# Kernel optimization log

Measured on AMD Instinct MI355X. Metric: run time of the kernel, lower is better.

Reference implementation:

```python
import jax, jax.numpy as jnp
import numpy as np

B, CIN, COUT, L, K, D = 64, 128, 256, 1024, 3, 2
P = (K - 1) * D  # causal padding = 4
THRESH = 0.1
SLOPE = 0.2  # LeakyReLU negative slope


def setup_inputs() -> dict:
    key = jax.random.key(0)
    ks = jax.random.split(key, 24)
    rn = lambda k, shape, s=0.05: jax.random.normal(k, shape, dtype=jnp.float32) * s
    return {
        "x": rn(ks[0], (B, CIN, L), 1.0),
        "conv1_w": rn(ks[1], (COUT, CIN, K)),
        "conv1_b": rn(ks[2], (COUT,)),
        "Wz_w": rn(ks[3], (COUT, COUT)), "Wz_b": rn(ks[4], (COUT,)),
        "Uz_w": rn(ks[5], (COUT, COUT)), "Uz_b": rn(ks[6], (COUT,)),
        "Wr_w": rn(ks[7], (COUT, COUT)), "Wr_b": rn(ks[8], (COUT,)),
        "Ur_w": rn(ks[9], (COUT, COUT)), "Ur_b": rn(ks[10], (COUT,)),
        "Wh_w": rn(ks[11], (COUT, COUT)), "Wh_b": rn(ks[12], (COUT,)),
        "Uh_w": rn(ks[13], (COUT, COUT)), "Uh_b": rn(ks[14], (COUT,)),
        "conv2_w": rn(ks[15], (COUT, COUT, K)),
        "conv2_b": rn(ks[16], (COUT,)),
        "skip_w": rn(ks[17], (COUT, CIN, 1)),
        "skip_b": rn(ks[18], (COUT,)),
        "aw": jnp.ones((1,), jnp.float32),  # AttentionZeroedLayer param, init ones
    }


def _causal_conv(x, w, b):
    # x: [B,C,L], w: [O,I,K]; pad both sides by P then chomp the right tail
    y = jax.lax.conv_general_dilated(
        x, w, window_strides=(1,), padding=[(P, P)], rhs_dilation=(D,),
        dimension_numbers=("NCH", "OIH", "NCH"))
    y = y + b[None, :, None]
    return y[:, :, :-P] if P > 0 else y


def reference(x, conv1_w, conv1_b, Wz_w, Wz_b, Uz_w, Uz_b, Wr_w, Wr_b,
              Ur_w, Ur_b, Wh_w, Wh_b, Uh_w, Uh_b, conv2_w, conv2_b,
              skip_w, skip_b, aw):
    res = x
    # conv1 -> chomp -> LeakyReLU (dropout=0, identity in eval)
    h1 = jax.nn.leaky_relu(_causal_conv(x, conv1_w, conv1_b), SLOPE)  # [B,COUT,L]
    xt = h1.transpose(0, 2, 1)  # [B,L,C]
    # precompute input-side GRU projections as batched GEMMs
    xz = jnp.einsum("blc,hc->blh", xt, Wz_w) + Wz_b
    xr = jnp.einsum("blc,hc->blh", xt, Wr_w) + Wr_b
    xh = jnp.einsum("blc,hc->blh", xt, Wh_w) + Wh_b

    def step(h, ins):
        xz_t, xr_t, xh_t = ins
        z = jax.nn.sigmoid(xz_t + h @ Uz_w.T + Uz_b)
        r = jax.nn.sigmoid(xr_t + h @ Ur_w.T + Ur_b)
        h_tilde = jnp.tanh(xh_t + r * (h @ Uh_w.T + Uh_b))
        h_new = (1 - z) * h + z * h_tilde
        return h_new, h_new

    h0 = jnp.zeros((B, COUT), x.dtype)
    _, hs = jax.lax.scan(step, h0, (xz.transpose(1, 0, 2),
                                    xr.transpose(1, 0, 2),
                                    xh.transpose(1, 0, 2)))  # [L,B,C]
    g = hs.transpose(1, 2, 0)  # [B,COUT,L]
    # AttentionZeroedLayer: zero elements with |g| < threshold * sigmoid(aw)
    gate = jax.nn.sigmoid(aw)[0]
    g = jnp.where(jnp.abs(g) < THRESH * gate, jnp.zeros_like(g), g)
    # conv2 -> chomp -> LeakyReLU
    y = jax.nn.leaky_relu(_causal_conv(g, conv2_w, conv2_b), SLOPE)
    # 1x1 skip connection (in_channels != out_channels)
    res = jax.lax.conv_general_dilated(
        res, skip_w, window_strides=(1,), padding=[(0, 0)],
        dimension_numbers=("NCH", "OIH", "NCH")) + skip_b[None, :, None]
    return y + res
```

## Files before the change

### kernel.cpp

```cpp
#include <hip/hip_runtime.h>
#include <hip/hip_bf16.h>


typedef _Float16 f16;
typedef _Float16 h2_t __attribute__((ext_vector_type(2)));

__device__ __forceinline__ float bf1(unsigned short s){ return __uint_as_float(((unsigned)s)<<16); }

__device__ __forceinline__ unsigned packh2(float a, float b){
  h2_t h; h[0] = (f16)a; h[1] = (f16)b;
  return *(unsigned*)&h;
}
__device__ __forceinline__ unsigned bf2h2(unsigned u){
  return packh2(bf1((unsigned short)(u & 0xffffu)), bf1((unsigned short)(u >> 16)));
}

__device__ __forceinline__ float fdot2(unsigned a, unsigned b, float c){
#if __has_builtin(__builtin_amdgcn_fdot2)
  return __builtin_amdgcn_fdot2(*(h2_t*)&a, *(h2_t*)&b, c, false);
#else
  h2_t x = *(h2_t*)&a, y = *(h2_t*)&b;
  return c + (float)x[0]*(float)y[0] + (float)x[1]*(float)y[1];
#endif
}

__device__ __forceinline__ unsigned short f2bf(float f){
  __hip_bfloat16 h = __float2bfloat16(f);
  return *(unsigned short*)&h;
}
__device__ __forceinline__ unsigned packbf2(float a, float b){
  return (unsigned)f2bf(a) | ((unsigned)f2bf(b)<<16);
}
__device__ __forceinline__ float h2lo(unsigned u){ h2_t h = *(h2_t*)&u; return (float)h[0]; }
__device__ __forceinline__ float h2hi(unsigned u){ h2_t h = *(h2_t*)&u; return (float)h[1]; }

__device__ __forceinline__ bool aw_is_f32(const void* aw){
  return ((const unsigned*)aw)[0] == 0x3F800000u;
}

__device__ __forceinline__ float dpp_add_b1(float v){
  int x = __builtin_amdgcn_update_dpp(0, __float_as_int(v), 0xB1, 0xF, 0xF, true);
  return v + __int_as_float(x);
}
__device__ __forceinline__ float dpp_add_4e(float v){
  int x = __builtin_amdgcn_update_dpp(0, __float_as_int(v), 0x4E, 0xF, 0xF, true);
  return v + __int_as_float(x);
}
__device__ __forceinline__ float red4(float v){
  return dpp_add_4e(dpp_add_b1(v));
}

__global__ void k_repack(const void* __restrict__ w1,  const void* __restrict__ w2,
                         const void* __restrict__ Wz,  const void* __restrict__ Wr,
                         const void* __restrict__ Wh,  const void* __restrict__ wsk,
                         const void* __restrict__ Uz,  const void* __restrict__ Ur,
                         const void* __restrict__ Uh,
                         const void* __restrict__ b1,  const void* __restrict__ Wzb,
                         const void* __restrict__ Wrb, const void* __restrict__ Whb,
                         const void* __restrict__ Uzb, const void* __restrict__ Urb,
                         const void* __restrict__ Uhb, const void* __restrict__ b2,
                         const void* __restrict__ bsk, const void* __restrict__ aw,
                         f16* __restrict__ p1, f16* __restrict__ p2,
                         f16* __restrict__ pz, f16* __restrict__ pr,
                         f16* __restrict__ ph, f16* __restrict__ ps,
                         f16* __restrict__ puz, f16* __restrict__ pur,
                         f16* __restrict__ puh, float* __restrict__ bc)
{
  const bool f32 = aw_is_f32(aw);
  auto G = [&](const void* p, int idx)->float{
    return f32 ? ((const float*)p)[idx] : bf1(((const unsigned short*)p)[idx]);
  };
  int i = blockIdx.x*256 + threadIdx.x;
  if (i < 196608){
    int t=i/65536, r=i%65536, cc=r>>11, r2=r&2047, o=r2>>3, ci=r2&7, c=cc*8+ci;
    p2[i] = (f16)G(w2, o*768 + c*3 + t);
  }
  if (i < 98304){
    int t=i/32768, r=i%32768, cc=r>>11, r2=r&2047, o=r2>>3, ci=r2&7, c=cc*8+ci;
    p1[i] = (f16)G(w1, o*384 + c*3 + t);
  }
  if (i < 65536){
    int cc=i>>11, r2=i&2047, o=r2>>3, ci=r2&7, c=cc*8+ci;
    int s = o*256 + c;
    pz[i]=(f16)G(Wz, s); pr[i]=(f16)G(Wr, s); ph[i]=(f16)G(Wh, s);
    puz[i]=(f16)G(Uz, i); pur[i]=(f16)G(Ur, i); puh[i]=(f16)G(Uh, i);
  }
  if (i < 32768){
    int cc=i>>11, r2=i&2047, o=r2>>3, ci=r2&7, c=cc*8+ci;
    ps[i]=(f16)G(wsk, o*128 + c);
  }
  if (i < 2304){
    int which = i>>8, j = i&255;
    const void* src[9] = {b1, Wzb, Wrb, Whb, Uzb, Urb, Uhb, b2, bsk};
    bc[i] = G(src[which], j);
  }
  if (i == 2304){
    float v = G(aw, 0);
    bc[2304] = 0.1f / (1.f + __expf(-v));
    bc[2305] = f32 ? 1.f : 0.f;
  }
}

__global__ __launch_bounds__(256,2) void k_conv1proj(
    const void* __restrict__ x,
    const f16* __restrict__ W1,
    const f16* __restrict__ WZ, const f16* __restrict__ WR, const f16* __restrict__ WH,
    const float* __restrict__ bc,
    f16* __restrict__ XZ, f16* __restrict__ XR, f16* __restrict__ XH,
    int Lc, int t0)
{
  __shared__ unsigned smem_u[12544];
  f16* xa = (f16*)smem_u;
  unsigned* tileA = smem_u + 4352;
  f16* hy = (f16*)(smem_u + 4352);
  const int b = blockIdx.y;
  const int lt = blockIdx.x*64;
  const int gl0 = t0 + lt;
  const int tid = threadIdx.x, lb = tid&7, ob = tid>>3;
  const bool f32 = (bc[2305] != 0.f);

  #pragma unroll
  for (int k=0;k<17;k++){
    int idx = tid + k*256;
    int c = idx/34, lp = idx - c*34;
    int gl = gl0 - 4 + lp*2;
    unsigned u = 0u;
    if (gl >= 0){
      if (f32){
        float2 v = *(const float2*)((const float*)x + ((size_t)b*128 + c)*1024 + gl);
        u = packh2(v.x, v.y);
      } else {
        u = bf2h2(*(const unsigned*)((const unsigned short*)x + ((size_t)b*128 + c)*1024 + gl));
      }
    }
    tileA[c*35 + lp] = u;
  }
  __syncthreads();
  #pragma unroll
  for (int k=0;k<17;k++){
    int idx = tid + k*256;
    int row = idx>>6, cp = idx&63;
    unsigned u0 = tileA[(2*cp)*35 + (row>>1)];
    unsigned u1 = tileA[(2*cp+1)*35 + (row>>1)];
    unsigned short s0 = (row&1)? (unsigned short)(u0>>16):(unsigned short)(u0&0xffffu);
    unsigned short s1 = (row&1)? (unsigned short)(u1>>16):(unsigned short)(u1&0xffffu);
    int sw = (cp>>2) ^ ((row>>3)&7);
    *(unsigned*)(&xa[row*128 + sw*8 + (cp&3)*2]) = (unsigned)s0 | ((unsigned)s1<<16);
  }
  __syncthreads();

  float acc[8][8];
  uint4 wreg[8], wnext[8];

  #pragma unroll
  for (int i=0;i<8;i++)
    #pragma unroll
    for (int j=0;j<8;j++) acc[i][j]=0.f;
  #pragma unroll
  for (int oi=0;oi<8;oi++) wreg[oi] = *(const uint4*)(W1 + ob*64 + oi*8);
  for (int ch=0; ch<48; ch++){
    if (ch+1 < 48){
      const f16* wn = W1 + (size_t)(ch+1)*2048 + ob*64;
      #pragma unroll
      for (int oi=0;oi<8;oi++) wnext[oi] = *(const uint4*)(wn + oi*8);
    }
    int t = ch>>4, cc = ch&15;
    #pragma unroll
    for (int li=0; li<8; li++){
      int row = lb*8 + li + t*2;
      int sw = cc ^ ((row>>3)&7);
      uint4 a = *(const uint4*)(&xa[row*128 + sw*8]);
      #pragma unroll
      for (int oi=0; oi<8; oi++){
        acc[li][oi] = fdot2(a.x, wreg[oi].x, acc[li][oi]);
        acc[li][oi] = fdot2(a.y, wreg[oi].y, acc[li][oi]);
        acc[li][oi] = fdot2(a.z, wreg[oi].z, acc[li][oi]);
        acc[li][oi] = fdot2(a.w, wreg[oi].w, acc[li][oi]);
      }
    }
    #pragma unroll
    for (int oi=0;oi<8;oi++) wreg[oi] = wnext[oi];
  }
  {
    const float* bp = bc + 0 + ob*8;
    #pragma unroll
    for (int li=0; li<8; li++){
      int row = lb*8 + li;
      f16 vals[8];
      #pragma unroll
      for (int oi=0;oi<8;oi++){
        float v = acc[li][oi] + bp[oi];
        vals[oi] = (f16)((v>0.f) ? v : 0.2f*v);
      }
      *(uint4*)(&hy[row*256 + ((ob ^ ((row>>3)&7))<<3)]) = *(uint4*)vals;
    }
  }
  __syncthreads();

  const f16* Wg[3] = {WZ, WR, WH};
  f16* Og[3] = {XZ, XR, XH};
  for (int g3=0; g3<3; g3++){
    const f16* Wp = Wg[g3];
    #pragma unroll
    for (int i=0;i<8;i++)
      #pragma unroll
      for (int j=0;j<8;j++) acc[i][j]=0.f;
    #pragma unroll
    for (int oi=0;oi<8;oi++) wreg[oi] = *(const uint4*)(Wp + ob*64 + oi*8);
    for (int ch=0; ch<32; ch++){
      if (ch+1 < 32){
        const f16* wn = Wp + (size_t)(ch+1)*2048 + ob*64;
        #pragma unroll
        for (int oi=0;oi<8;oi++) wnext[oi] = *(const uint4*)(wn + oi*8);
      }
      #pragma unroll
      for (int li=0; li<8; li++){
        int row = lb*8 + li;
        int sw = ch ^ ((row>>3)&7);
        uint4 a = *(const uint4*)(&hy[row*256 + sw*8]);
        #pragma unroll
        for (int oi=0; oi<8; oi++){
          acc[li][oi] = fdot2(a.x, wreg[oi].x, acc[li][oi]);
          acc[li][oi] = fdot2(a.y, wreg[oi].y, acc[li][oi]);
          acc[li][oi] = fdot2(a.z, wreg[oi].z, acc[li][oi]);
          acc[li][oi] = fdot2(a.w, wreg[oi].w, acc[li][oi]);
        }
      }
      #pragma unroll
      for (int oi=0;oi<8;oi++) wreg[oi] = wnext[oi];
    }
    f16* Ob = Og[g3] + ((size_t)b*Lc + lt)*256 + ob*8;
    #pragma unroll
    for (int li=0; li<8; li++){
      f16 vals[8];
      #pragma unroll
      for (int oi=0;oi<8;oi++){
        int o = ob*8 + oi;
        float bias = bc[256 + g3*256 + o] + ((g3<2) ? bc[1024 + g3*256 + o] : 0.f);
        vals[oi] = (f16)(acc[li][oi] + bias);
      }
      *(uint4*)(Ob + (size_t)(lb*8 + li)*256) = *(uint4*)vals;
    }
  }
}

__global__ __launch_bounds__(512)
__attribute__((amdgpu_waves_per_eu(2,2)))
void k_scan(
    const f16* __restrict__ XZ, const f16* __restrict__ XR, const f16* __restrict__ XH,
    const f16* __restrict__ pUz, const f16* __restrict__ pUr, const f16* __restrict__ pUh,
    const float* __restrict__ bc,
    f16* __restrict__ G, float* __restrict__ carry,
    int Lc, int first)
{
  const int b = blockIdx.x, tid = threadIdx.x;
  const int kp = tid&3, grp = tid>>2, r0 = grp*2;
  __shared__ unsigned hb[2][160];

  {
    f16* gb = G + (size_t)b*(Lc+4)*256;
    int row = tid>>7, col = tid&127;
    unsigned v = 0u;
    if (!first) v = *(unsigned*)(gb + (size_t)(Lc+row)*256 + col*2);
    *(unsigned*)(gb + (size_t)row*256 + col*2) = v;
  }

  unsigned uz0[32],uz1[32],ur0[32],ur1[32],uh0[32],uh1[32];
  const int cbase = kp*64;
  #pragma unroll
  for (int j4=0;j4<8;j4++){
    uint4 q;
    q = *(const uint4*)(pUz + r0*256     + cbase + j4*8);
    uz0[j4*4+0]=q.x; uz0[j4*4+1]=q.y; uz0[j4*4+2]=q.z; uz0[j4*4+3]=q.w;
    q = *(const uint4*)(pUz + (r0+1)*256 + cbase + j4*8);
    uz1[j4*4+0]=q.x; uz1[j4*4+1]=q.y; uz1[j4*4+2]=q.z; uz1[j4*4+3]=q.w;
    q = *(const uint4*)(pUr + r0*256     + cbase + j4*8);
    ur0[j4*4+0]=q.x; ur0[j4*4+1]=q.y; ur0[j4*4+2]=q.z; ur0[j4*4+3]=q.w;
    q = *(const uint4*)(pUr + (r0+1)*256 + cbase + j4*8);
    ur1[j4*4+0]=q.x; ur1[j4*4+1]=q.y; ur1[j4*4+2]=q.z; ur1[j4*4+3]=q.w;
    q = *(const uint4*)(pUh + r0*256     + cbase + j4*8);
    uh0[j4*4+0]=q.x; uh0[j4*4+1]=q.y; uh0[j4*4+2]=q.z; uh0[j4*4+3]=q.w;
    q = *(const uint4*)(pUh + (r0+1)*256 + cbase + j4*8);
    uh1[j4*4+0]=q.x; uh1[j4*4+1]=q.y; uh1[j4*4+2]=q.z; uh1[j4*4+3]=q.w;
  }
  const float bh0=bc[1536+r0], bh1=bc[1536+r0+1];
  const float thr = bc[2304];
  float hp0, hp1;
  if (first){ hp0 = 0.f; hp1 = 0.f; }
  else { hp0 = carry[b*256 + r0]; hp1 = carry[b*256 + r0 + 1]; }
  const int wslot = (grp>>5)*40 + (grp&31);
  if (kp == 0) hb[0][wslot] = packh2(hp0, hp1);

  const f16* xzp = XZ + (size_t)b*Lc*256 + r0;
  const f16* xrp = XR + (size_t)b*Lc*256 + r0;
  const f16* xhp = XH + (size_t)b*Lc*256 + r0;
  f16* gp = G + (size_t)b*(Lc+4)*256 + r0;

  unsigned xzv = *(const unsigned*)(xzp);
  unsigned xrv = *(const unsigned*)(xrp);
  unsigned xhv = *(const unsigned*)(xhp);
  __syncthreads();

  for (int t=0; t<Lc; t++){
    const int tn = (t+1 < Lc) ? t+1 : t;
    const unsigned nz = *(const unsigned*)(xzp + (size_t)tn*256);
    const unsigned nr = *(const unsigned*)(xrp + (size_t)tn*256);
    const unsigned nh = *(const unsigned*)(xhp + (size_t)tn*256);

    const unsigned* hbr = hb[t&1] + kp*40;
    float az0=0,az1=0,ar0=0,ar1=0,ah0=0,ah1=0;
    #pragma unroll
    for (int j4=0;j4<8;j4++){
      const uint4 hv = *(const uint4*)(hbr + j4*4);
      const unsigned hw[4] = {hv.x, hv.y, hv.z, hv.w};
      #pragma unroll
      for (int p=0;p<4;p++){
        const int J = j4*4+p;
        az0 = fdot2(hw[p], uz0[J], az0);
        az1 = fdot2(hw[p], uz1[J], az1);
        ar0 = fdot2(hw[p], ur0[J], ar0);
        ar1 = fdot2(hw[p], ur1[J], ar1);
        ah0 = fdot2(hw[p], uh0[J], ah0);
        ah1 = fdot2(hw[p], uh1[J], ah1);
      }
    }
    az0 = red4(az0); az1 = red4(az1);
    ar0 = red4(ar0); ar1 = red4(ar1);
    ah0 = red4(ah0); ah1 = red4(ah1);

    const float z0  = 1.f/(1.f+__expf(-(h2lo(xzv)+az0)));
    const float z1  = 1.f/(1.f+__expf(-(h2hi(xzv)+az1)));
    const float rr0 = 1.f/(1.f+__expf(-(h2lo(xrv)+ar0)));
    const float rr1 = 1.f/(1.f+__expf(-(h2hi(xrv)+ar1)));
    const float e0  = __expf(2.f*(h2lo(xhv)+rr0*(ah0+bh0)));
    const float e1  = __expf(2.f*(h2hi(xhv)+rr1*(ah1+bh1)));
    const float hh0 = 1.f - 2.f/(e0+1.f);
    const float hh1 = 1.f - 2.f/(e1+1.f);
    const float hn0 = (1.f-z0)*hp0 + z0*hh0;
    const float hn1 = (1.f-z1)*hp1 + z1*hh1;
    hp0 = hn0; hp1 = hn1;
    if (kp == 0){
      const float g0 = (fabsf(hn0) < thr) ? 0.f : hn0;
      const float g1 = (fabsf(hn1) < thr) ? 0.f : hn1;
      *(unsigned*)(gp + (size_t)(t+4)*256) = packh2(g0, g1);
      hb[(t+1)&1][wslot] = packh2(hn0, hn1);
    }
    xzv = nz; xrv = nr; xhv = nh;
    __syncthreads();
  }
  if (kp == 0){
    carry[b*256 + r0]     = hp0;
    carry[b*256 + r0 + 1] = hp1;
  }
}

__global__ __launch_bounds__(256,2) void k_final(const f16* __restrict__ G,
    const void* __restrict__ x, const f16* __restrict__ W2,
    const f16* __restrict__ WS, const float* __restrict__ bc,
    void* __restrict__ out, int Lc, int t0)
{
  __shared__ unsigned smem2[8704];
  f16* atG = (f16*)smem2;
  const int b = blockIdx.y;
  const int lt = blockIdx.x*64;
  const int gl0 = t0 + lt;
  const int tid = threadIdx.x, lb = tid&7, ob = tid>>3;
  const bool f32 = (bc[2305] != 0.f);

  {
    const f16* Ab = G + (size_t)b*(Lc+4)*256 + (size_t)lt*256;
    for (int idx=tid; idx<68*32; idx+=256){
      int row = idx>>5, cc = idx&31;
      uint4 v = *(const uint4*)(Ab + (size_t)row*256 + cc*8);
      *(uint4*)(&atG[row*256 + ((cc ^ ((row>>3)&7))<<3)]) = v;
    }
  }
  __syncthreads();

  float acc[8][8];
  #pragma unroll
  for (int i=0;i<8;i++)
    #pragma unroll
    for (int j=0;j<8;j++) acc[i][j]=0.f;

  uint4 wreg[8], wnext[8];
  #pragma unroll
  for (int oi=0;oi<8;oi++) wreg[oi] = *(const uint4*)(W2 + ob*64 + oi*8);
  for (int ch=0; ch<96; ch++){
    if (ch+1 < 96){
      const f16* wn = W2 + (size_t)(ch+1)*2048 + ob*64;
      #pragma unroll
      for (int oi=0;oi<8;oi++) wnext[oi] = *(const uint4*)(wn + oi*8);
    }
    int t = ch>>5, cc = ch&31;
    #pragma unroll
    for (int li=0; li<8; li++){
      int row = lb*8 + li + t*2;
      uint4 a = *(const uint4*)(&atG[row*256 + ((cc ^ ((row>>3)&7))<<3)]);
      #pragma unroll
      for (int oi=0; oi<8; oi++){
        acc[li][oi] = fdot2(a.x, wreg[oi].x, acc[li][oi]);
        acc[li][oi] = fdot2(a.y, wreg[oi].y, acc[li][oi]);
        acc[li][oi] = fdot2(a.z, wreg[oi].z, acc[li][oi]);
        acc[li][oi] = fdot2(a.w, wreg[oi].w, acc[li][oi]);
      }
    }
    #pragma unroll
    for (int oi=0;oi<8;oi++) wreg[oi] = wnext[oi];
  }
  {
    const float* bp = bc + 1792 + ob*8;
    #pragma unroll
    for (int li=0;li<8;li++)
      #pragma unroll
      for (int oi=0;oi<8;oi++){
        float v = acc[li][oi] + bp[oi];
        acc[li][oi] = (v>0.f) ? v : 0.2f*v;
      }
  }
  __syncthreads();

  unsigned* tileB = smem2;
  f16* xa2 = (f16*)(smem2 + 4352);
  #pragma unroll
  for (int k=0;k<16;k++){
    int idx = tid + k*256;
    int c = idx>>5, lp = idx&31;
    unsigned u;
    if (f32){
      float2 v = *(const float2*)((const float*)x + ((size_t)b*128 + c)*1024 + gl0 + lp*2);
      u = packh2(v.x, v.y);
    } else {
      u = bf2h2(*(const unsigned*)((const unsigned short*)x + ((size_t)b*128 + c)*1024 + gl0 + lp*2));
    }
    tileB[c*33 + lp] = u;
  }
  __syncthreads();
  #pragma unroll
  for (int k=0;k<16;k++){
    int idx = tid + k*256;
    int row = idx>>6, cp = idx&63;
    unsigned u0 = tileB[(2*cp)*33 + (row>>1)];
    unsigned u1 = tileB[(2*cp+1)*33 + (row>>1)];
    unsigned short s0 = (row&1)? (unsigned short)(u0>>16):(unsigned short)(u0&0xffffu);
    unsigned short s1 = (row&1)? (unsigned short)(u1>>16):(unsigned short)(u1&0xffffu);
    int sw = (cp>>2) ^ ((row>>3)&7);
    *(unsigned*)(&xa2[row*128 + sw*8 + (cp&3)*2]) = (unsigned)s0 | ((unsigned)s1<<16);
  }
  __syncthreads();

  #pragma unroll
  for (int oi=0;oi<8;oi++) wreg[oi] = *(const uint4*)(WS + ob*64 + oi*8);
  for (int ch=0; ch<16; ch++){
    if (ch+1 < 16){
      const f16* wn = WS + (size_t)(ch+1)*2048 + ob*64;
      #pragma unroll
      for (int oi=0;oi<8;oi++) wnext[oi] = *(const uint4*)(wn + oi*8);
    }
    #pragma unroll
    for (int li=0; li<8; li++){
      int row = lb*8 + li;
      int sw = ch ^ ((row>>3)&7);
      uint4 a = *(const uint4*)(&xa2[row*128 + sw*8]);
      #pragma unroll
      for (int oi=0; oi<8; oi++){
        acc[li][oi] = fdot2(a.x, wreg[oi].x, acc[li][oi]);
        acc[li][oi] = fdot2(a.y, wreg[oi].y, acc[li][oi]);
        acc[li][oi] = fdot2(a.z, wreg[oi].z, acc[li][oi]);
        acc[li][oi] = fdot2(a.w, wreg[oi].w, acc[li][oi]);
      }
    }
    #pragma unroll
    for (int oi=0;oi<8;oi++) wreg[oi] = wnext[oi];
  }
  {
    const float* sp = bc + 2048 + ob*8;
    #pragma unroll
    for (int oi=0;oi<8;oi++){
      int o = ob*8 + oi;
      size_t base = ((size_t)b*256 + o)*1024 + gl0 + lb*8;
      if (f32){
        float st[8];
        #pragma unroll
        for (int j=0;j<8;j++) st[j] = acc[j][oi] + sp[oi];
        *(uint4*)((float*)out + base)     = *(uint4*)&st[0];
        *(uint4*)((float*)out + base + 4) = *(uint4*)&st[4];
      } else {
        unsigned st[4];
        #pragma unroll
        for (int j=0;j<4;j++)
          st[j] = packbf2(acc[2*j][oi] + sp[oi], acc[2*j+1][oi] + sp[oi]);
        *(uint4*)((unsigned short*)out + base) = *(uint4*)st;
      }
    }
  }
}

extern "C" void kernel_launch(void* const* d_in, const int* in_sizes, int n_in,
                              void* d_out, int out_size, void* d_ws, size_t ws_size,
                              hipStream_t stream)
{
  const void* x   = d_in[0];
  const void* w1  = d_in[1];
  const void* b1  = d_in[2];
  const void* Wz  = d_in[3];
  const void* Wzb = d_in[4];
  const void* Uz  = d_in[5];
  const void* Uzb = d_in[6];
  const void* Wr  = d_in[7];
  const void* Wrb = d_in[8];
  const void* Ur  = d_in[9];
  const void* Urb = d_in[10];
  const void* Wh  = d_in[11];
  const void* Whb = d_in[12];
  const void* Uh  = d_in[13];
  const void* Uhb = d_in[14];
  const void* w2  = d_in[15];
  const void* b2  = d_in[16];
  const void* wsk = d_in[17];
  const void* bsk = d_in[18];
  const void* aw  = d_in[19];

  auto need = [](long long Lc)->size_t{
    return (size_t)(2LL*(758784LL + 3LL*64*Lc*256 + 64LL*(Lc+4)*256));
  };
  int Lc = 1024;
  if (ws_size < need(1024)) Lc = 256;
  if (ws_size < need(256))  Lc = 64;
  const int NCH = 1024 / Lc;

  f16* W = (f16*)d_ws;
  f16*   w1p   = W;
  f16*   w2p   = W + 98304;
  f16*   wzp   = W + 294912;
  f16*   wrp   = W + 360448;
  f16*   whp   = W + 425984;
  f16*   wsp   = W + 491520;
  f16*   uzp   = W + 524288;
  f16*   urp   = W + 589824;
  f16*   uhp   = W + 655360;
  float* bc    = (float*)(W + 720896);
  float* carry = (float*)(W + 726016);
  f16*   xz    = W + 758784;
  f16*   xr    = xz + (size_t)64*Lc*256;
  f16*   xh    = xr + (size_t)64*Lc*256;
  f16*   g     = xh + (size_t)64*Lc*256;

  k_repack<<<dim3(768), 256, 0, stream>>>(w1, w2, Wz, Wr, Wh, wsk, Uz, Ur, Uh,
                                          b1, Wzb, Wrb, Whb, Uzb, Urb, Uhb, b2,
                                          bsk, aw,
                                          w1p, w2p, wzp, wrp, whp, wsp,
                                          uzp, urp, uhp, bc);
  for (int c = 0; c < NCH; c++){
    const int t0 = c * Lc;
    const int first = (c == 0) ? 1 : 0;
    k_conv1proj<<<dim3(Lc/64,64), 256, 0, stream>>>(x, w1p, wzp, wrp, whp, bc,
                                                    xz, xr, xh, Lc, t0);
    k_scan<<<dim3(64), 512, 0, stream>>>(xz, xr, xh, uzp, urp, uhp, bc,
                                         g, carry, Lc, first);
    k_final<<<dim3(Lc/64,64), 256, 0, stream>>>(g, x, w2p, wsp, bc,
                                                d_out, Lc, t0);
  }
}
```

Measured before the change: 2.196 ms.

## Fuse conv1, scan and final into one launch with cross-chunk software pipelining

Merges the three per-chunk kernels into one kernel whose blocks take different roles. The sequential GRU scan for chunk c runs alongside conv1/projection for chunk c+1 and the final conv for chunk c-1, using double-buffered projection and G buffers. The aim is to keep the GPU busy while the latency-bound 64-block scan runs. It also drops the register double-buffered weight prefetch and changes the chunk size to 256. The cost is larger workspace, more launches, and 512-thread blocks for the GEMM roles that compete with the scan for compute units.

```diff
diff --git a/kernel.cpp b/kernel.cpp
--- a/kernel.cpp
+++ b/kernel.cpp
@@ -101,7 +101,8 @@
   }
 }
 
-__global__ __launch_bounds__(256,2) void k_conv1proj(
+__device__ __forceinline__ void role_conv1(
+    unsigned* smAll, int tid, int pb,
     const void* __restrict__ x,
     const f16* __restrict__ W1,
     const f16* __restrict__ WZ, const f16* __restrict__ WR, const f16* __restrict__ WH,
@@ -109,19 +110,20 @@
     f16* __restrict__ XZ, f16* __restrict__ XR, f16* __restrict__ XH,
     int Lc, int t0)
 {
-  __shared__ unsigned smem_u[12544];
+  unsigned* smem_u = smAll + (tid>>8)*12544;
   f16* xa = (f16*)smem_u;
   unsigned* tileA = smem_u + 4352;
   f16* hy = (f16*)(smem_u + 4352);
-  const int b = blockIdx.y;
-  const int lt = blockIdx.x*64;
+  const int tt = pb*2 + (tid>>8);
+  const int b = tt & 63;
+  const int lt = (tt>>6)*64;
   const int gl0 = t0 + lt;
-  const int tid = threadIdx.x, lb = tid&7, ob = tid>>3;
+  const int t8 = tid & 255, lb = t8&7, ob = t8>>3;
   const bool f32 = (bc[2305] != 0.f);
 
   #pragma unroll
   for (int k=0;k<17;k++){
-    int idx = tid + k*256;
+    int idx = t8 + k*256;
     int c = idx/34, lp = idx - c*34;
     int gl = gl0 - 4 + lp*2;
     unsigned u = 0u;
@@ -138,7 +140,7 @@
   __syncthreads();
   #pragma unroll
   for (int k=0;k<17;k++){
-    int idx = tid + k*256;
+    int idx = t8 + k*256;
     int row = idx>>6, cp = idx&63;
     unsigned u0 = tileA[(2*cp)*35 + (row>>1)];
     unsigned u1 = tileA[(2*cp+1)*35 + (row>>1)];
@@ -150,20 +152,15 @@
   __syncthreads();
 
   float acc[8][8];
-  uint4 wreg[8], wnext[8];
+  uint4 wreg[8];
 
   #pragma unroll
   for (int i=0;i<8;i++)
     #pragma unroll
     for (int j=0;j<8;j++) acc[i][j]=0.f;
-  #pragma unroll
-  for (int oi=0;oi<8;oi++) wreg[oi] = *(const uint4*)(W1 + ob*64 + oi*8);
   for (int ch=0; ch<48; ch++){
-    if (ch+1 < 48){
-      const f16* wn = W1 + (size_t)(ch+1)*2048 + ob*64;
-      #pragma unroll
-      for (int oi=0;oi<8;oi++) wnext[oi] = *(const uint4*)(wn + oi*8);
-    }
+    #pragma unroll
+    for (int oi=0;oi<8;oi++) wreg[oi] = *(const uint4*)(W1 + (size_t)ch*2048 + ob*64 + oi*8);
     int t = ch>>4, cc = ch&15;
     #pragma unroll
     for (int li=0; li<8; li++){
@@ -178,8 +175,6 @@
         acc[li][oi] = fdot2(a.w, wreg[oi].w, acc[li][oi]);
       }
     }
-    #pragma unroll
-    for (int oi=0;oi<8;oi++) wreg[oi] = wnext[oi];
   }
   {
     const float* bp = bc + 0 + ob*8;
@@ -205,14 +200,9 @@
     for (int i=0;i<8;i++)
       #pragma unroll
       for (int j=0;j<8;j++) acc[i][j]=0.f;
-    #pragma unroll
-    for (int oi=0;oi<8;oi++) wreg[oi] = *(const uint4*)(Wp + ob*64 + oi*8);
     for (int ch=0; ch<32; ch++){
-      if (ch+1 < 32){
-        const f16* wn = Wp + (size_t)(ch+1)*2048 + ob*64;
-        #pragma unroll
-        for (int oi=0;oi<8;oi++) wnext[oi] = *(const uint4*)(wn + oi*8);
-      }
+      #pragma unroll
+      for (int oi=0;oi<8;oi++) wreg[oi] = *(const uint4*)(Wp + (size_t)ch*2048 + ob*64 + oi*8);
       #pragma unroll
       for (int li=0; li<8; li++){
         int row = lb*8 + li;
@@ -226,8 +216,6 @@
           acc[li][oi] = fdot2(a.w, wreg[oi].w, acc[li][oi]);
         }
       }
-      #pragma unroll
-      for (int oi=0;oi<8;oi++) wreg[oi] = wnext[oi];
     }
     f16* Ob = Og[g3] + ((size_t)b*Lc + lt)*256 + ob*8;
     #pragma unroll
@@ -244,25 +232,26 @@
   }
 }
 
-__global__ __launch_bounds__(512)
-__attribute__((amdgpu_waves_per_eu(2,2)))
-void k_scan(
+__device__ __forceinline__ void role_scan(
+    unsigned* smem, int tid,
     const f16* __restrict__ XZ, const f16* __restrict__ XR, const f16* __restrict__ XH,
     const f16* __restrict__ pUz, const f16* __restrict__ pUr, const f16* __restrict__ pUh,
     const float* __restrict__ bc,
-    f16* __restrict__ G, float* __restrict__ carry,
+    f16* __restrict__ G, const f16* __restrict__ GP, float* __restrict__ carry,
     int Lc, int first)
 {
-  const int b = blockIdx.x, tid = threadIdx.x;
+  const int b = blockIdx.x;
   const int kp = tid&3, grp = tid>>2, r0 = grp*2;
-  __shared__ unsigned hb[2][160];
+  unsigned* hb0 = smem;
+  unsigned* hb1 = smem + 160;
 
   {
-    f16* gb = G + (size_t)b*(Lc+4)*256;
+    f16* gw = G + (size_t)b*(Lc+4)*256;
+    const f16* gr = GP + (size_t)b*(Lc+4)*256;
     int row = tid>>7, col = tid&127;
     unsigned v = 0u;
-    if (!first) v = *(unsigned*)(gb + (size_t)(Lc+row)*256 + col*2);
-    *(unsigned*)(gb + (size_t)row*256 + col*2) = v;
+    if (!first) v = *(const unsigned*)(gr + (size_t)(Lc+row)*256 + col*2);
+    *(unsigned*)(gw + (size_t)row*256 + col*2) = v;
   }
 
   unsigned uz0[32],uz1[32],ur0[32],ur1[32],uh0[32],uh1[32];
@@ -289,7 +278,7 @@
   if (first){ hp0 = 0.f; hp1 = 0.f; }
   else { hp0 = carry[b*256 + r0]; hp1 = carry[b*256 + r0 + 1]; }
   const int wslot = (grp>>5)*40 + (grp&31);
-  if (kp == 0) hb[0][wslot] = packh2(hp0, hp1);
+  if (kp == 0) hb0[wslot] = packh2(hp0, hp1);
 
   const f16* xzp = XZ + (size_t)b*Lc*256 + r0;
   const f16* xrp = XR + (size_t)b*Lc*256 + r0;
@@ -307,7 +296,7 @@
     const unsigned nr = *(const unsigned*)(xrp + (size_t)tn*256);
     const unsigned nh = *(const unsigned*)(xhp + (size_t)tn*256);
 
-    const unsigned* hbr = hb[t&1] + kp*40;
+    const unsigned* hbr = ((t&1) ? hb1 : hb0) + kp*40;
     float az0=0,az1=0,ar0=0,ar1=0,ah0=0,ah1=0;
     #pragma unroll
     for (int j4=0;j4<8;j4++){
@@ -343,7 +332,7 @@
       const float g0 = (fabsf(hn0) < thr) ? 0.f : hn0;
       const float g1 = (fabsf(hn1) < thr) ? 0.f : hn1;
       *(unsigned*)(gp + (size_t)(t+4)*256) = packh2(g0, g1);
-      hb[(t+1)&1][wslot] = packh2(hn0, hn1);
+      ((t&1) ? hb0 : hb1)[wslot] = packh2(hn0, hn1);
     }
     xzv = nz; xrv = nr; xhv = nh;
     __syncthreads();
@@ -354,22 +343,25 @@
   }
 }
 
-__global__ __launch_bounds__(256,2) void k_final(const f16* __restrict__ G,
-    const void* __restrict__ x, const f16* __restrict__ W2,
-    const f16* __restrict__ WS, const float* __restrict__ bc,
-    void* __restrict__ out, int Lc, int t0)
+__device__ __forceinline__ void role_final(
+    unsigned* smAll, int tid, int fb,
+    const f16* __restrict__ G, const void* __restrict__ x,
+    const f16* __restrict__ W2, const f16* __restrict__ WS,
+    const float* __restrict__ bc, void* __restrict__ out,
+    int Lc, int t0)
 {
-  __shared__ unsigned smem2[8704];
+  unsigned* smem2 = smAll + (tid>>8)*8704;
   f16* atG = (f16*)smem2;
-  const int b = blockIdx.y;
-  const int lt = blockIdx.x*64;
+  const int tt = fb*2 + (tid>>8);
+  const int b = tt & 63;
+  const int lt = (tt>>6)*64;
   const int gl0 = t0 + lt;
-  const int tid = threadIdx.x, lb = tid&7, ob = tid>>3;
+  const int t8 = tid & 255, lb = t8&7, ob = t8>>3;
   const bool f32 = (bc[2305] != 0.f);
 
   {
     const f16* Ab = G + (size_t)b*(Lc+4)*256 + (size_t)lt*256;
-    for (int idx=tid; idx<68*32; idx+=256){
+    for (int idx=t8; idx<68*32; idx+=256){
       int row = idx>>5, cc = idx&31;
       uint4 v = *(const uint4*)(Ab + (size_t)row*256 + cc*8);
       *(uint4*)(&atG[row*256 + ((cc ^ ((row>>3)&7))<<3)]) = v;
@@ -383,15 +375,10 @@
     #pragma unroll
     for (int j=0;j<8;j++) acc[i][j]=0.f;
 
-  uint4 wreg[8], wnext[8];
-  #pragma unroll
-  for (int oi=0;oi<8;oi++) wreg[oi] = *(const uint4*)(W2 + ob*64 + oi*8);
+  uint4 wreg[8];
   for (int ch=0; ch<96; ch++){
-    if (ch+1 < 96){
-      const f16* wn = W2 + (size_t)(ch+1)*2048 + ob*64;
-      #pragma unroll
-      for (int oi=0;oi<8;oi++) wnext[oi] = *(const uint4*)(wn + oi*8);
-    }
+    #pragma unroll
+    for (int oi=0;oi<8;oi++) wreg[oi] = *(const uint4*)(W2 + (size_t)ch*2048 + ob*64 + oi*8);
     int t = ch>>5, cc = ch&31;
     #pragma unroll
     for (int li=0; li<8; li++){
@@ -405,8 +392,6 @@
         acc[li][oi] = fdot2(a.w, wreg[oi].w, acc[li][oi]);
       }
     }
-    #pragma unroll
-    for (int oi=0;oi<8;oi++) wreg[oi] = wnext[oi];
   }
   {
     const float* bp = bc + 1792 + ob*8;
@@ -424,7 +409,7 @@
   f16* xa2 = (f16*)(smem2 + 4352);
   #pragma unroll
   for (int k=0;k<16;k++){
-    int idx = tid + k*256;
+    int idx = t8 + k*256;
     int c = idx>>5, lp = idx&31;
     unsigned u;
     if (f32){
@@ -438,7 +423,7 @@
   __syncthreads();
   #pragma unroll
   for (int k=0;k<16;k++){
-    int idx = tid + k*256;
+    int idx = t8 + k*256;
     int row = idx>>6, cp = idx&63;
     unsigned u0 = tileB[(2*cp)*33 + (row>>1)];
     unsigned u1 = tileB[(2*cp+1)*33 + (row>>1)];
@@ -449,14 +434,9 @@
   }
   __syncthreads();
 
-  #pragma unroll
-  for (int oi=0;oi<8;oi++) wreg[oi] = *(const uint4*)(WS + ob*64 + oi*8);
   for (int ch=0; ch<16; ch++){
-    if (ch+1 < 16){
-      const f16* wn = WS + (size_t)(ch+1)*2048 + ob*64;
-      #pragma unroll
-      for (int oi=0;oi<8;oi++) wnext[oi] = *(const uint4*)(wn + oi*8);
-    }
+    #pragma unroll
+    for (int oi=0;oi<8;oi++) wreg[oi] = *(const uint4*)(WS + (size_t)ch*2048 + ob*64 + oi*8);
     #pragma unroll
     for (int li=0; li<8; li++){
       int row = lb*8 + li;
@@ -470,8 +450,6 @@
         acc[li][oi] = fdot2(a.w, wreg[oi].w, acc[li][oi]);
       }
     }
-    #pragma unroll
-    for (int oi=0;oi<8;oi++) wreg[oi] = wnext[oi];
   }
   {
     const float* sp = bc + 2048 + ob*8;
@@ -494,6 +472,41 @@
       }
     }
   }
+}
+
+__global__ __launch_bounds__(512) void k_fused(
+    const void* __restrict__ x,
+    const f16* __restrict__ W1,
+    const f16* __restrict__ WZ, const f16* __restrict__ WR, const f16* __restrict__ WH,
+    const f16* __restrict__ W2, const f16* __restrict__ WS,
+    const f16* __restrict__ pUz, const f16* __restrict__ pUr, const f16* __restrict__ pUh,
+    const float* __restrict__ bc, void* __restrict__ out,
+    f16* __restrict__ xzA, f16* __restrict__ xrA, f16* __restrict__ xhA,
+    const f16* __restrict__ xzS, const f16* __restrict__ xrS, const f16* __restrict__ xhS,
+    f16* __restrict__ gS, const f16* __restrict__ gPrev,
+    float* __restrict__ carry,
+    int Lc, int t0P, int t0F, int first,
+    int haveS, int haveP, int haveF)
+{
+  __shared__ __align__(16) unsigned smem[25088];
+  const int tid = threadIdx.x;
+  int bid = blockIdx.x;
+  if (bid < 64){
+    if (haveS)
+      role_scan(smem, tid, xzS, xrS, xhS, pUz, pUr, pUh, bc, gS, gPrev, carry,
+                Lc, first);
+    return;
+  }
+  bid -= 64;
+  const int PB = Lc >> 1;
+  if (bid < PB){
+    if (haveP)
+      role_conv1(smem, tid, bid, x, W1, WZ, WR, WH, bc, xzA, xrA, xhA, Lc, t0P);
+    return;
+  }
+  bid -= PB;
+  if (haveF)
+    role_final(smem, tid, bid, gPrev, x, W2, WS, bc, out, Lc, t0F);
 }
 
 extern "C" void kernel_launch(void* const* d_in, const int* in_sizes, int n_in,
@@ -521,12 +534,13 @@
   const void* bsk = d_in[18];
   const void* aw  = d_in[19];
 
-  auto need = [](long long Lc)->size_t{
-    return (size_t)(2LL*(758784LL + 3LL*64*Lc*256 + 64LL*(Lc+4)*256));
-  };
-  int Lc = 1024;
-  if (ws_size < need(1024)) Lc = 256;
-  if (ws_size < need(256))  Lc = 64;
+  int Lc = 256;
+  {
+    auto need = [](long long L)->size_t{
+      return (size_t)(2LL*758784LL + 2LL*(6LL*64*L*256 + 2LL*64*(L+4)*256));
+    };
+    if (ws_size < need(256)) Lc = 64;
+  }
   const int NCH = 1024 / Lc;
 
   f16* W = (f16*)d_ws;
@@ -541,24 +555,41 @@
   f16*   uhp   = W + 655360;
   float* bc    = (float*)(W + 720896);
   float* carry = (float*)(W + 726016);
-  f16*   xz    = W + 758784;
-  f16*   xr    = xz + (size_t)64*Lc*256;
-  f16*   xh    = xr + (size_t)64*Lc*256;
-  f16*   g     = xh + (size_t)64*Lc*256;
+  const size_t S1 = (size_t)64*Lc*256;
+  const size_t G1 = (size_t)64*(Lc+4)*256;
+  f16* p = W + 758784;
+  f16* xzb[2] = {p,        p + 3*S1};
+  f16* xrb[2] = {p + S1,   p + 4*S1};
+  f16* xhb[2] = {p + 2*S1, p + 5*S1};
+  f16* gbuf[2] = {p + 6*S1, p + 6*S1 + G1};
 
   k_repack<<<dim3(768), 256, 0, stream>>>(w1, w2, Wz, Wr, Wh, wsk, Uz, Ur, Uh,
                                           b1, Wzb, Wrb, Whb, Uzb, Urb, Uhb, b2,
                                           bsk, aw,
                                           w1p, w2p, wzp, wrp, whp, wsp,
                                           uzp, urp, uhp, bc);
+  const dim3 grid(64 + Lc);
+  k_fused<<<grid, 512, 0, stream>>>(x, w1p, wzp, wrp, whp, w2p, wsp,
+      uzp, urp, uhp, bc, d_out,
+      xzb[0], xrb[0], xhb[0],
+      xzb[0], xrb[0], xhb[0],
+      gbuf[0], gbuf[1], carry,
+      Lc, 0, 0, 1, 0, 1, 0);
   for (int c = 0; c < NCH; c++){
-    const int t0 = c * Lc;
-    const int first = (c == 0) ? 1 : 0;
-    k_conv1proj<<<dim3(Lc/64,64), 256, 0, stream>>>(x, w1p, wzp, wrp, whp, bc,
-                                                    xz, xr, xh, Lc, t0);
-    k_scan<<<dim3(64), 512, 0, stream>>>(xz, xr, xh, uzp, urp, uhp, bc,
-                                         g, carry, Lc, first);
-    k_final<<<dim3(Lc/64,64), 256, 0, stream>>>(g, x, w2p, wsp, bc,
-                                                d_out, Lc, t0);
-  }
-}
+    const int pp = (c+1)&1, cp = c&1;
+    const int fpar = (c >= 1) ? ((c-1)&1) : 1;
+    k_fused<<<grid, 512, 0, stream>>>(x, w1p, wzp, wrp, whp, w2p, wsp,
+        uzp, urp, uhp, bc, d_out,
+        xzb[pp], xrb[pp], xhb[pp],
+        xzb[cp], xrb[cp], xhb[cp],
+        gbuf[cp], gbuf[fpar], carry,
+        Lc, (c+1)*Lc, (c-1)*Lc, (c==0)?1:0,
+        1, (c+1<NCH)?1:0, (c>=1)?1:0);
+  }
+  k_fused<<<grid, 512, 0, stream>>>(x, w1p, wzp, wrp, whp, w2p, wsp,
+      uzp, urp, uhp, bc, d_out,
+      xzb[0], xrb[0], xhb[0],
+      xzb[0], xrb[0], xhb[0],
+      gbuf[0], gbuf[(NCH-1)&1], carry,
+      Lc, 0, (NCH-1)*Lc, 0, 0, 0, 1);
+}
```

Result: faster. 1.837 ms (-16.3%).
